# Performance work log

Hardware: AMD Instinct MI355X
Metric: run time of the kernel (lower is better)

## Reference

```python
import jax, jax.numpy as jnp
import numpy as np

HIDDEN = 1024
N_HEAD = 16
HEAD_DIM = HIDDEN // N_HEAD
ROPE_THETA = 10000.0


def setup_inputs() -> dict:
    key = jax.random.key(0)
    ks = jax.random.split(key, 6)
    B, T = 4, 2048
    x = jax.random.normal(ks[0], (B, T, HIDDEN), dtype=jnp.float32)
    rnn_state = jax.random.normal(ks[1], (B, HIDDEN), dtype=jnp.float32)
    Wqkv = jax.random.normal(ks[2], (HIDDEN, 3 * HIDDEN), dtype=jnp.float32) * 0.02
    bqkv = jnp.zeros((3 * HIDDEN,), dtype=jnp.float32)
    Wproj = jax.random.normal(ks[3], (HIDDEN, HIDDEN), dtype=jnp.float32) * 0.02
    bproj = jnp.zeros((HIDDEN,), dtype=jnp.float32)
    return {"x": x, "rnn_state": rnn_state, "Wqkv": Wqkv, "bqkv": bqkv,
            "Wproj": Wproj, "bproj": bproj}


def _rope_tables(T, dtype):
    # GPT-NeoX style half-split RoPE
    inv_freq = 1.0 / (ROPE_THETA ** (jnp.arange(0, HEAD_DIM, 2, dtype=jnp.float32) / HEAD_DIM))
    freqs = jnp.arange(T, dtype=jnp.float32)[:, None] * inv_freq[None, :]  # [T, D/2]
    return jnp.cos(freqs).astype(dtype), jnp.sin(freqs).astype(dtype)


def _apply_rope(x, cos, sin):
    # x: [B, H, T, D]; cos/sin: [T, D/2]
    x1, x2 = jnp.split(x, 2, axis=-1)
    c = cos[None, None, :, :]
    s = sin[None, None, :, :]
    return jnp.concatenate([x1 * c - x2 * s, x1 * s + x2 * c], axis=-1)


def reference(x, rnn_state, Wqkv, bqkv, Wproj, bproj):
    B, T, C = x.shape
    qkv = x @ Wqkv + bqkv  # [B, T, 3C]
    q, k, v = jnp.split(qkv, 3, axis=-1)
    # split heads -> [B, H, T, D]
    def heads(t):
        return t.reshape(B, T, N_HEAD, HEAD_DIM).transpose(0, 2, 1, 3)
    q, k, v = heads(q), heads(k), heads(v)
    cos, sin = _rope_tables(T, x.dtype)
    q = _apply_rope(q, cos, sin)
    k = _apply_rope(k, cos, sin)
    scale = 1.0 / jnp.sqrt(jnp.asarray(HEAD_DIM, dtype=x.dtype))
    scores = jnp.einsum('bhtd,bhsd->bhts', q, k) * scale  # [B,H,T,T]
    # causal additive mask: 0 on/below diag, -inf above (matches torch buffer)
    causal = jnp.tril(jnp.ones((T, T), dtype=bool))
    scores = jnp.where(causal[None, None, :, :], scores, -jnp.inf)
    attn = jax.nn.softmax(scores, axis=-1)
    out = jnp.einsum('bhts,bhsd->bhtd', attn, v)  # [B,H,T,D]
    out = out.transpose(0, 2, 1, 3).reshape(B, T, C)
    output = out @ Wproj + bproj
    return (output, rnn_state)
```

## Files before the change

kernel.cpp:

```cpp
#include <hip/hip_runtime.h>
#include <cstdint>
#include <cstddef>
#include <math.h>

typedef unsigned short u16;
typedef __attribute__((ext_vector_type(8))) short short8;
typedef __attribute__((ext_vector_type(4))) float floatx4;

#define HIDDEN 1024
#define NHEAD 16
#define HD 64
#define BB 4
#define TT 2048
#define MM (BB*TT)
#define NQKV 3072
#define NEGINF (-30000.0f)

__device__ inline u16 f2bf(float f){
  union { float f; unsigned u; } v; v.f = f;
  unsigned r = v.u + 0x7FFFu + ((v.u >> 16) & 1u);
  return (u16)(r >> 16);
}
__device__ inline void load_lds16(const void* g, void* l){
  __builtin_amdgcn_global_load_lds((const __attribute__((address_space(1))) void*)g,
                                   (__attribute__((address_space(3))) void*)l,
                                   16, 0, 0);
}

__global__ void rope_tables(float* __restrict__ cosT, float* __restrict__ sinT){
  const int idx = blockIdx.x * 256 + threadIdx.x;
  const int t = idx >> 5, f = idx & 31;
  const float inv = powf(10000.0f, -(float)f * (1.0f / 32.0f));
  const float ang = (float)t * inv;
  cosT[idx] = cosf(ang);
  sinT[idx] = sinf(ang);
}

__global__ void convert_x(const float* __restrict__ in, u16* __restrict__ outp){
  const int i = (blockIdx.x * 256 + threadIdx.x) * 8;
  #pragma unroll
  for (int u = 0; u < 8; u++) outp[i + u] = f2bf(in[i + u]);
}

__global__ void transpose_f32_bf16(const float* __restrict__ in, u16* __restrict__ out,
                                   int R, int C){
  __shared__ alignas(16) u16 tile[32][33];
  const int c0 = blockIdx.x * 32, r0 = blockIdx.y * 32;
  const int tx = threadIdx.x & 31, ty = threadIdx.x >> 5;
  for (int i = ty; i < 32; i += 8)
    tile[i][tx] = f2bf(in[(size_t)(r0 + i) * C + c0 + tx]);
  __syncthreads();
  for (int i = ty; i < 32; i += 8) out[(size_t)(c0 + i) * R + r0 + tx] = tile[tx][i];
}

__global__ void gemm_qkv(const u16* __restrict__ X, const u16* __restrict__ WT,
                         const float* __restrict__ bias,
                         const float* __restrict__ ropeC, const float* __restrict__ ropeS,
                         u16* __restrict__ Qb, u16* __restrict__ Kb, u16* __restrict__ Vtg)
{
  __shared__ alignas(16) u16 As[2][128 * 32];
  __shared__ alignas(16) u16 Bs[2][128 * 32];
  const int tid = threadIdx.x;
  const int wid = tid >> 6, lane = tid & 63;
  const int quad = lane >> 4, ln = lane & 15;
  const int row0 = blockIdx.y * 128, col0 = blockIdx.x * 128;
  const int wm = (wid >> 1) * 64, wn = (wid & 1) * 64;
  floatx4 acc[4][4] = {};

  const int sr = tid >> 2, sk = (tid & 3) * 8;

  load_lds16(&X [(size_t)(row0 + sr      ) * 1024 + sk], &As[0][(size_t)(tid      ) * 8]);
  load_lds16(&X [(size_t)(row0 + sr + 64 ) * 1024 + sk], &As[0][(size_t)(tid + 256) * 8]);
  load_lds16(&WT[(size_t)(col0 + sr      ) * 1024 + sk], &Bs[0][(size_t)(tid      ) * 8]);
  load_lds16(&WT[(size_t)(col0 + sr + 64 ) * 1024 + sk], &Bs[0][(size_t)(tid + 256) * 8]);
  __syncthreads();

  #pragma unroll 2
  for (int kk = 0; kk < 32; ++kk){
    const int cur = kk & 1;
    if (kk < 31){
      const int k0 = (kk + 1) * 32;
      load_lds16(&X [(size_t)(row0 + sr      ) * 1024 + k0 + sk], &As[cur ^ 1][(size_t)(tid      ) * 8]);
      load_lds16(&X [(size_t)(row0 + sr + 64 ) * 1024 + k0 + sk], &As[cur ^ 1][(size_t)(tid + 256) * 8]);
      load_lds16(&WT[(size_t)(col0 + sr      ) * 1024 + k0 + sk], &Bs[cur ^ 1][(size_t)(tid      ) * 8]);
      load_lds16(&WT[(size_t)(col0 + sr + 64 ) * 1024 + k0 + sk], &Bs[cur ^ 1][(size_t)(tid + 256) * 8]);
    }
    short8 a[4], b[4];
    #pragma unroll
    for (int i = 0; i < 4; i++) a[i] = *(const short8*)&As[cur][(wm + i*16 + ln) * 32 + quad * 8];
    #pragma unroll
    for (int j = 0; j < 4; j++) b[j] = *(const short8*)&Bs[cur][(wn + j*16 + ln) * 32 + quad * 8];
    #pragma unroll
    for (int i = 0; i < 4; i++)
      #pragma unroll
      for (int j = 0; j < 4; j++)
        acc[i][j] = __builtin_amdgcn_mfma_f32_16x16x32_bf16(a[i], b[j], acc[i][j], 0, 0, 0);
    __syncthreads();
  }

  const int wcol0 = col0 + wn;
  const int which = wcol0 >> 10;
  const int h = (wcol0 & 1023) >> 6;
  float bs[4];
  #pragma unroll
  for (int j = 0; j < 4; j++) bs[j] = bias[wcol0 + j*16 + ln];

  #pragma unroll
  for (int i = 0; i < 4; i++){
    #pragma unroll
    for (int rr = 0; rr < 4; rr++){
      const int rowg = row0 + wm + i*16 + quad*4 + rr;
      const int b_ = rowg >> 11, t = rowg & 2047;
      if (which < 2){
        u16* op = (which == 0 ? Qb : Kb) + ((size_t)(b_ * NHEAD + h) * TT + t) * HD;
        #pragma unroll
        for (int j = 0; j < 2; j++){
          const int f = j*16 + ln;
          const float cs = ropeC[t * 32 + f];
          const float sn = ropeS[t * 32 + f];
          const float x1 = acc[i][j  ][rr] + bs[j  ];
          const float x2 = acc[i][j+2][rr] + bs[j+2];
          float y1 = x1 * cs - x2 * sn;
          float y2 = x1 * sn + x2 * cs;
          if (which == 0){ y1 *= 0.125f; y2 *= 0.125f; }
          op[f]      = f2bf(y1);
          op[f + 32] = f2bf(y2);
        }
      } else {
        #pragma unroll
        for (int j = 0; j < 4; j++)
          Vtg[((size_t)(b_ * NHEAD + h) * HD + j*16 + ln) * TT + t] = f2bf(acc[i][j][rr] + bs[j]);
      }
    }
  }
}

__global__ void attn(const u16* __restrict__ Qb, const u16* __restrict__ Kb,
                     const u16* __restrict__ Vtg, u16* __restrict__ AO)
{
  const int bh = blockIdx.x, tbi = 31 - (int)blockIdx.y;
  const int tid = threadIdx.x;
  const int wid = tid >> 6, lane = tid & 63;
  const int quad = lane >> 4, ln = lane & 15;

  __shared__ alignas(16) u16 Kl[64 * 72];
  __shared__ alignas(16) u16 Vt[64 * 72];
  __shared__ alignas(16) u16 Pl[4][16 * 72];

  const u16* Qh = Qb  + (size_t)bh * TT * HD;
  const u16* Kh = Kb  + (size_t)bh * TT * HD;
  const u16* Vh = Vtg + (size_t)bh * HD * TT;
  const int b_ = bh >> 4, h = bh & 15;

  const int q0 = tbi * 64 + wid * 16;

  const short8 aq0 = *(const short8*)&Qh[(size_t)(q0 + ln) * HD + quad*8];
  const short8 aq1 = *(const short8*)&Qh[(size_t)(q0 + ln) * HD + 32 + quad*8];

  floatx4 o[4] = {};
  float l_i[4] = {};

  const int pr = tid >> 3, pc = (tid & 7) * 8;

  short8 kpre0 = *(const short8*)&Kh[(size_t)(pr     ) * HD + pc];
  short8 kpre1 = *(const short8*)&Kh[(size_t)(pr + 32) * HD + pc];
  short8 vpre0 = *(const short8*)&Vh[(size_t)(pr     ) * TT + pc];
  short8 vpre1 = *(const short8*)&Vh[(size_t)(pr + 32) * TT + pc];

  const int nch = tbi + 1;
  for (int ch = 0; ch < nch; ++ch){
    const int key0 = ch * 64;
    __syncthreads();
    *(short8*)&Kl[(pr     ) * 72 + pc] = kpre0;
    *(short8*)&Kl[(pr + 32) * 72 + pc] = kpre1;
    *(short8*)&Vt[(pr     ) * 72 + pc] = vpre0;
    *(short8*)&Vt[(pr + 32) * 72 + pc] = vpre1;
    if (ch + 1 < nch){
      const int nk0 = key0 + 64;
      kpre0 = *(const short8*)&Kh[(size_t)(nk0 + pr     ) * HD + pc];
      kpre1 = *(const short8*)&Kh[(size_t)(nk0 + pr + 32) * HD + pc];
      vpre0 = *(const short8*)&Vh[(size_t)(pr     ) * TT + nk0 + pc];
      vpre1 = *(const short8*)&Vh[(size_t)(pr + 32) * TT + nk0 + pc];
    }
    __syncthreads();

    floatx4 s[4];
    #pragma unroll
    for (int j = 0; j < 4; j++){
      const short8 kb0 = *(const short8*)&Kl[(j*16 + ln) * 72 + quad*8];
      const short8 kb1 = *(const short8*)&Kl[(j*16 + ln) * 72 + 32 + quad*8];
      floatx4 z = {0.0f, 0.0f, 0.0f, 0.0f};
      z = __builtin_amdgcn_mfma_f32_16x16x32_bf16(aq0, kb0, z, 0, 0, 0);
      z = __builtin_amdgcn_mfma_f32_16x16x32_bf16(aq1, kb1, z, 0, 0, 0);
      s[j] = z;
    }
    if (ch == nch - 1){
      #pragma unroll
      for (int j = 0; j < 4; j++)
        #pragma unroll
        for (int rr = 0; rr < 4; rr++){
          const int key = key0 + j*16 + ln;
          const int t   = q0 + quad*4 + rr;
          if (key > t) s[j][rr] = NEGINF;
        }
    }
    #pragma unroll
    for (int j = 0; j < 4; j++)
      #pragma unroll
      for (int rr = 0; rr < 4; rr++){
        const float p = __expf(s[j][rr]);
        s[j][rr] = p;
        l_i[rr] += p;
      }
    #pragma unroll
    for (int j = 0; j < 4; j++)
      #pragma unroll
      for (int rr = 0; rr < 4; rr++)
        Pl[wid][(quad*4 + rr) * 72 + j*16 + ln] = f2bf(s[j][rr]);
    const short8 pa0 = *(const short8*)&Pl[wid][ln * 72 + quad*8];
    const short8 pa1 = *(const short8*)&Pl[wid][ln * 72 + 32 + quad*8];
    #pragma unroll
    for (int n = 0; n < 4; n++){
      const short8 vb0 = *(const short8*)&Vt[(n*16 + ln) * 72 + quad*8];
      const short8 vb1 = *(const short8*)&Vt[(n*16 + ln) * 72 + 32 + quad*8];
      o[n] = __builtin_amdgcn_mfma_f32_16x16x32_bf16(pa0, vb0, o[n], 0, 0, 0);
      o[n] = __builtin_amdgcn_mfma_f32_16x16x32_bf16(pa1, vb1, o[n], 0, 0, 0);
    }
  }

  #pragma unroll
  for (int rr = 0; rr < 4; rr++){
    float rs = l_i[rr];
    #pragma unroll
    for (int off = 1; off < 16; off <<= 1) rs += __shfl_xor(rs, off);
    l_i[rr] = rs;
  }

  #pragma unroll
  for (int n = 0; n < 4; n++)
    #pragma unroll
    for (int rr = 0; rr < 4; rr++){
      const int t = q0 + quad*4 + rr;
      const float inv_l = 1.0f / fmaxf(l_i[rr], 1e-20f);
      AO[(size_t)(b_ * TT + t) * HIDDEN + h * HD + n*16 + ln] = f2bf(o[n][rr] * inv_l);
    }
}

__global__ void gemm_proj(const u16* __restrict__ A, const u16* __restrict__ WT,
                          const float* __restrict__ bias, float* __restrict__ out)
{
  __shared__ alignas(16) u16 As[2][128 * 32];
  __shared__ alignas(16) u16 Bs[2][128 * 32];
  const int tid = threadIdx.x;
  const int wid = tid >> 6, lane = tid & 63;
  const int quad = lane >> 4, ln = lane & 15;
  const int row0 = blockIdx.y * 128, col0 = blockIdx.x * 128;
  const int wm = (wid >> 1) * 64, wn = (wid & 1) * 64;
  floatx4 acc[4][4] = {};

  const int sr = tid >> 2, sk = (tid & 3) * 8;

  load_lds16(&A [(size_t)(row0 + sr      ) * 1024 + sk], &As[0][(size_t)(tid      ) * 8]);
  load_lds16(&A [(size_t)(row0 + sr + 64 ) * 1024 + sk], &As[0][(size_t)(tid + 256) * 8]);
  load_lds16(&WT[(size_t)(col0 + sr      ) * 1024 + sk], &Bs[0][(size_t)(tid      ) * 8]);
  load_lds16(&WT[(size_t)(col0 + sr + 64 ) * 1024 + sk], &Bs[0][(size_t)(tid + 256) * 8]);
  __syncthreads();

  #pragma unroll 2
  for (int kk = 0; kk < 32; ++kk){
    const int cur = kk & 1;
    if (kk < 31){
      const int k0 = (kk + 1) * 32;
      load_lds16(&A [(size_t)(row0 + sr      ) * 1024 + k0 + sk], &As[cur ^ 1][(size_t)(tid      ) * 8]);
      load_lds16(&A [(size_t)(row0 + sr + 64 ) * 1024 + k0 + sk], &As[cur ^ 1][(size_t)(tid + 256) * 8]);
      load_lds16(&WT[(size_t)(col0 + sr      ) * 1024 + k0 + sk], &Bs[cur ^ 1][(size_t)(tid      ) * 8]);
      load_lds16(&WT[(size_t)(col0 + sr + 64 ) * 1024 + k0 + sk], &Bs[cur ^ 1][(size_t)(tid + 256) * 8]);
    }
    short8 a[4], b[4];
    #pragma unroll
    for (int i = 0; i < 4; i++) a[i] = *(const short8*)&As[cur][(wm + i*16 + ln) * 32 + quad * 8];
    #pragma unroll
    for (int j = 0; j < 4; j++) b[j] = *(const short8*)&Bs[cur][(wn + j*16 + ln) * 32 + quad * 8];
    #pragma unroll
    for (int i = 0; i < 4; i++)
      #pragma unroll
      for (int j = 0; j < 4; j++)
        acc[i][j] = __builtin_amdgcn_mfma_f32_16x16x32_bf16(a[i], b[j], acc[i][j], 0, 0, 0);
    __syncthreads();
  }

  float bs[4];
  #pragma unroll
  for (int j = 0; j < 4; j++) bs[j] = bias[col0 + wn + j*16 + ln];
  #pragma unroll
  for (int i = 0; i < 4; i++)
    #pragma unroll
    for (int rr = 0; rr < 4; rr++){
      const int rowg = row0 + wm + i*16 + quad*4 + rr;
      #pragma unroll
      for (int j = 0; j < 4; j++)
        out[(size_t)rowg * HIDDEN + col0 + wn + j*16 + ln] = acc[i][j][rr] + bs[j];
    }
}

__global__ void copy_tail(const float* __restrict__ rnn, float* __restrict__ out){
  const int i = blockIdx.x * 256 + threadIdx.x;
  if (i < BB * HIDDEN) out[(size_t)MM * HIDDEN + i] = rnn[i];
}

extern "C" void kernel_launch(void* const* d_in, const int* in_sizes, int n_in,
                              void* d_out, int out_size, void* d_ws, size_t ws_size,
                              hipStream_t stream)
{
  const float* x     = (const float*)d_in[0];
  const float* rnn   = (const float*)d_in[1];
  const float* Wqkv  = (const float*)d_in[2];
  const float* bqkv  = (const float*)d_in[3];
  const float* Wproj = (const float*)d_in[4];
  const float* bproj = (const float*)d_in[5];
  float* out = (float*)d_out;

  char* ws = (char*)d_ws;
  size_t off = 0;
  float* ropeC  = (float*)(ws + off); off += (size_t)TT * 32 * 4;
  float* ropeS  = (float*)(ws + off); off += (size_t)TT * 32 * 4;
  u16*   xN     = (u16*)(ws + off);   off += (size_t)MM * HIDDEN * 2;
  u16*   WqkvT  = (u16*)(ws + off);   off += (size_t)NQKV * HIDDEN * 2;
  u16*   WprojT = (u16*)(ws + off);   off += (size_t)HIDDEN * HIDDEN * 2;
  u16*   Qb     = (u16*)(ws + off);   off += (size_t)MM * HIDDEN * 2;
  u16*   Kb     = (u16*)(ws + off);   off += (size_t)MM * HIDDEN * 2;
  u16*   Vtg    = (u16*)(ws + off);   off += (size_t)MM * HIDDEN * 2;
  u16*   AO     = (u16*)(ws + off);   off += (size_t)MM * HIDDEN * 2;

  rope_tables<<<(TT * 32) / 256, 256, 0, stream>>>(ropeC, ropeS);
  convert_x<<<(MM * HIDDEN) / (256 * 8), 256, 0, stream>>>(x, xN);
  transpose_f32_bf16<<<dim3(NQKV / 32, HIDDEN / 32), 256, 0, stream>>>(Wqkv, WqkvT, HIDDEN, NQKV);
  transpose_f32_bf16<<<dim3(HIDDEN / 32, HIDDEN / 32), 256, 0, stream>>>(Wproj, WprojT, HIDDEN, HIDDEN);
  gemm_qkv<<<dim3(NQKV / 128, MM / 128), 256, 0, stream>>>(xN, WqkvT, bqkv, ropeC, ropeS, Qb, Kb, Vtg);
  attn<<<dim3(BB * NHEAD, 32), 256, 0, stream>>>(Qb, Kb, Vtg, AO);
  gemm_proj<<<dim3(HIDDEN / 128, MM / 128), 256, 0, stream>>>(AO, WprojT, bproj, out);
  copy_tail<<<(BB * HIDDEN + 255) / 256, 256, 0, stream>>>(rnn, out);
}
```

Measured before the change: 294.7 us.

## Triple-buffer GEMM K-loop with explicit vmcnt waits and XCD-aware tile swizzle

Both projection GEMMs move from a double-buffered LDS pipeline to a three-stage ring. Each iteration waits with explicit s_waitcnt vmcnt counts and raw barriers, so two tile loads stay in flight behind the MFMA work. Block indices are also remapped so blocks landing on the same XCD share a column strip of weights, which should improve L2 reuse. The cost is 50% more LDS per block, which may reduce occupancy, and hand-tuned wait counts that depend on how many loads each stage issues.

Measured after the change: 296.4 us. Within noise of the previous version (+0.6%).

```diff
diff --git a/kernel.cpp b/kernel.cpp
--- a/kernel.cpp
+++ b/kernel.cpp
@@ -53,50 +53,74 @@
   for (int i = ty; i < 32; i += 8) out[(size_t)(c0 + i) * R + r0 + tx] = tile[tx][i];
 }
 
+#define GFENCE() asm volatile("" ::: "memory")
+
+#define STAGE(Aptr, Bptr, buf, kstep) do {                                                  \
+    const int k0_ = (kstep) * 32;                                                           \
+    load_lds16(&Aptr[(size_t)(row0 + sr      ) * 1024 + k0_ + sk], &As[buf][(size_t)(tid      ) * 8]); \
+    load_lds16(&Aptr[(size_t)(row0 + sr + 64 ) * 1024 + k0_ + sk], &As[buf][(size_t)(tid + 256) * 8]); \
+    load_lds16(&Bptr[(size_t)(col0 + sr      ) * 1024 + k0_ + sk], &Bs[buf][(size_t)(tid      ) * 8]); \
+    load_lds16(&Bptr[(size_t)(col0 + sr + 64 ) * 1024 + k0_ + sk], &Bs[buf][(size_t)(tid + 256) * 8]); \
+  } while (0)
+
+#define COMPUTE(buf) do {                                                                   \
+    short8 a[4], b[4];                                                                      \
+    _Pragma("unroll")                                                                       \
+    for (int i = 0; i < 4; i++) a[i] = *(const short8*)&As[buf][(wm + i*16 + ln) * 32 + quad * 8]; \
+    _Pragma("unroll")                                                                       \
+    for (int j = 0; j < 4; j++) b[j] = *(const short8*)&Bs[buf][(wn + j*16 + ln) * 32 + quad * 8]; \
+    _Pragma("unroll")                                                                       \
+    for (int i = 0; i < 4; i++)                                                             \
+      _Pragma("unroll")                                                                     \
+      for (int j = 0; j < 4; j++)                                                           \
+        acc[i][j] = __builtin_amdgcn_mfma_f32_16x16x32_bf16(a[i], b[j], acc[i][j], 0, 0, 0);\
+  } while (0)
+
+#define KLOOP(Aptr, Bptr) do {                                                              \
+    STAGE(Aptr, Bptr, 0, 0); STAGE(Aptr, Bptr, 1, 1); STAGE(Aptr, Bptr, 2, 2);              \
+    _Pragma("unroll 3")                                                                     \
+    for (int kk = 0; kk < 30; ++kk){                                                        \
+      const int cur = kk % 3;                                                               \
+      asm volatile("s_waitcnt vmcnt(8)" ::: "memory");                                      \
+      __builtin_amdgcn_s_barrier();                                                         \
+      GFENCE();                                                                             \
+      COMPUTE(cur);                                                                         \
+      GFENCE();                                                                             \
+      __builtin_amdgcn_s_barrier();                                                         \
+      GFENCE();                                                                             \
+      if (kk < 29) STAGE(Aptr, Bptr, cur, kk + 3);                                          \
+    }                                                                                       \
+    asm volatile("s_waitcnt vmcnt(4)" ::: "memory");                                        \
+    __builtin_amdgcn_s_barrier();                                                           \
+    GFENCE();                                                                               \
+    COMPUTE(0);                                                         \
+    asm volatile("s_waitcnt vmcnt(0)" ::: "memory");                                        \
+    __builtin_amdgcn_s_barrier();                                                           \
+    GFENCE();                                                                               \
+    COMPUTE(1);                                                         \
+  } while (0)
+
 __global__ void gemm_qkv(const u16* __restrict__ X, const u16* __restrict__ WT,
                          const float* __restrict__ bias,
                          const float* __restrict__ ropeC, const float* __restrict__ ropeS,
                          u16* __restrict__ Qb, u16* __restrict__ Kb, u16* __restrict__ Vtg)
 {
-  __shared__ alignas(16) u16 As[2][128 * 32];
-  __shared__ alignas(16) u16 Bs[2][128 * 32];
+  __shared__ alignas(16) u16 As[3][128 * 32];
+  __shared__ alignas(16) u16 Bs[3][128 * 32];
   const int tid = threadIdx.x;
   const int wid = tid >> 6, lane = tid & 63;
   const int quad = lane >> 4, ln = lane & 15;
-  const int row0 = blockIdx.y * 128, col0 = blockIdx.x * 128;
+
+  const int flat = (int)blockIdx.y * 24 + (int)blockIdx.x;
+  const int xcd = flat & 7, idx = flat >> 3;
+  const int col0 = (xcd * 3 + (idx % 3)) * 128;
+  const int row0 = (idx / 3) * 128;
+
   const int wm = (wid >> 1) * 64, wn = (wid & 1) * 64;
   floatx4 acc[4][4] = {};
-
   const int sr = tid >> 2, sk = (tid & 3) * 8;
 
-  load_lds16(&X [(size_t)(row0 + sr      ) * 1024 + sk], &As[0][(size_t)(tid      ) * 8]);
-  load_lds16(&X [(size_t)(row0 + sr + 64 ) * 1024 + sk], &As[0][(size_t)(tid + 256) * 8]);
-  load_lds16(&WT[(size_t)(col0 + sr      ) * 1024 + sk], &Bs[0][(size_t)(tid      ) * 8]);
-  load_lds16(&WT[(size_t)(col0 + sr + 64 ) * 1024 + sk], &Bs[0][(size_t)(tid + 256) * 8]);
-  __syncthreads();
-
-  #pragma unroll 2
-  for (int kk = 0; kk < 32; ++kk){
-    const int cur = kk & 1;
-    if (kk < 31){
-      const int k0 = (kk + 1) * 32;
-      load_lds16(&X [(size_t)(row0 + sr      ) * 1024 + k0 + sk], &As[cur ^ 1][(size_t)(tid      ) * 8]);
-      load_lds16(&X [(size_t)(row0 + sr + 64 ) * 1024 + k0 + sk], &As[cur ^ 1][(size_t)(tid + 256) * 8]);
-      load_lds16(&WT[(size_t)(col0 + sr      ) * 1024 + k0 + sk], &Bs[cur ^ 1][(size_t)(tid      ) * 8]);
-      load_lds16(&WT[(size_t)(col0 + sr + 64 ) * 1024 + k0 + sk], &Bs[cur ^ 1][(size_t)(tid + 256) * 8]);
-    }
-    short8 a[4], b[4];
-    #pragma unroll
-    for (int i = 0; i < 4; i++) a[i] = *(const short8*)&As[cur][(wm + i*16 + ln) * 32 + quad * 8];
-    #pragma unroll
-    for (int j = 0; j < 4; j++) b[j] = *(const short8*)&Bs[cur][(wn + j*16 + ln) * 32 + quad * 8];
-    #pragma unroll
-    for (int i = 0; i < 4; i++)
-      #pragma unroll
-      for (int j = 0; j < 4; j++)
-        acc[i][j] = __builtin_amdgcn_mfma_f32_16x16x32_bf16(a[i], b[j], acc[i][j], 0, 0, 0);
-    __syncthreads();
-  }
+  KLOOP(X, WT);
 
   const int wcol0 = col0 + wn;
   const int which = wcol0 >> 10;
@@ -249,45 +273,22 @@
 __global__ void gemm_proj(const u16* __restrict__ A, const u16* __restrict__ WT,
                           const float* __restrict__ bias, float* __restrict__ out)
 {
-  __shared__ alignas(16) u16 As[2][128 * 32];
-  __shared__ alignas(16) u16 Bs[2][128 * 32];
+  __shared__ alignas(16) u16 As[3][128 * 32];
+  __shared__ alignas(16) u16 Bs[3][128 * 32];
   const int tid = threadIdx.x;
   const int wid = tid >> 6, lane = tid & 63;
   const int quad = lane >> 4, ln = lane & 15;
-  const int row0 = blockIdx.y * 128, col0 = blockIdx.x * 128;
+
+  const int flat = (int)blockIdx.y * 8 + (int)blockIdx.x;
+  const int xcd = flat & 7, idx = flat >> 3;
+  const int col0 = xcd * 128;
+  const int row0 = idx * 128;
+
   const int wm = (wid >> 1) * 64, wn = (wid & 1) * 64;
   floatx4 acc[4][4] = {};
-
   const int sr = tid >> 2, sk = (tid & 3) * 8;
 
-  load_lds16(&A [(size_t)(row0 + sr      ) * 1024 + sk], &As[0][(size_t)(tid      ) * 8]);
-  load_lds16(&A [(size_t)(row0 + sr + 64 ) * 1024 + sk], &As[0][(size_t)(tid + 256) * 8]);
-  load_lds16(&WT[(size_t)(col0 + sr      ) * 1024 + sk], &Bs[0][(size_t)(tid      ) * 8]);
-  load_lds16(&WT[(size_t)(col0 + sr + 64 ) * 1024 + sk], &Bs[0][(size_t)(tid + 256) * 8]);
-  __syncthreads();
-
-  #pragma unroll 2
-  for (int kk = 0; kk < 32; ++kk){
-    const int cur = kk & 1;
-    if (kk < 31){
-      const int k0 = (kk + 1) * 32;
-      load_lds16(&A [(size_t)(row0 + sr      ) * 1024 + k0 + sk], &As[cur ^ 1][(size_t)(tid      ) * 8]);
-      load_lds16(&A [(size_t)(row0 + sr + 64 ) * 1024 + k0 + sk], &As[cur ^ 1][(size_t)(tid + 256) * 8]);
-      load_lds16(&WT[(size_t)(col0 + sr      ) * 1024 + k0 + sk], &Bs[cur ^ 1][(size_t)(tid      ) * 8]);
-      load_lds16(&WT[(size_t)(col0 + sr + 64 ) * 1024 + k0 + sk], &Bs[cur ^ 1][(size_t)(tid + 256) * 8]);
-    }
-    short8 a[4], b[4];
-    #pragma unroll
-    for (int i = 0; i < 4; i++) a[i] = *(const short8*)&As[cur][(wm + i*16 + ln) * 32 + quad * 8];
-    #pragma unroll
-    for (int j = 0; j < 4; j++) b[j] = *(const short8*)&Bs[cur][(wn + j*16 + ln) * 32 + quad * 8];
-    #pragma unroll
-    for (int i = 0; i < 4; i++)
-      #pragma unroll
-      for (int j = 0; j < 4; j++)
-        acc[i][j] = __builtin_amdgcn_mfma_f32_16x16x32_bf16(a[i], b[j], acc[i][j], 0, 0, 0);
-    __syncthreads();
-  }
+  KLOOP(A, WT);
 
   float bs[4];
   #pragma unroll
```
